# Optimization experiments

Hardware: AMD Instinct MI355X
Metric: run time of the kernel (lower is better)

The kernel has to match this reference:

```python
import jax, jax.numpy as jnp
import numpy as np

# static config (mirrors params)
T, B, NA, NF = 48, 256, 23, 4
D = NA * NF          # y_dim = 92
XD = 2               # x_dim
H = 128              # rnn_dim
HD = 128             # h_dim
NL = 2               # n_layers
FS = 0.1
BURN = 12
IN_ENC = XD + D + H  # GRU input size = 222
A0, A1 = 12, 11      # agents 0..11 -> net0, 12..22 -> net1


def setup_inputs() -> dict:
    key = jax.random.key(0)
    ks = jax.random.split(key, 16)
    s = 0.05
    rn = lambda k, shape: jax.random.normal(k, shape, jnp.float32) * s
    return {
        "states": jax.random.normal(ks[0], (T + 1, 1, B, D), jnp.float32),
        # per-network (leading dim 2) GRU layer-0 and layer-1 weights (torch GRU layout: [r|z|n])
        "W_ih0": rn(ks[1], (2, 3 * H, IN_ENC)),
        "W_hh0": rn(ks[2], (2, 3 * H, H)),
        "b_ih0": rn(ks[3], (2, 3 * H)),
        "b_hh0": rn(ks[4], (2, 3 * H)),
        "W_ih1": rn(ks[5], (2, 3 * H, H)),
        "W_hh1": rn(ks[6], (2, 3 * H, H)),
        "b_ih1": rn(ks[7], (2, 3 * H)),
        "b_hh1": rn(ks[8], (2, 3 * H)),
        # decoder MLP (dropout is identity in eval) + mean head
        "W1": rn(ks[9], (2, HD, H)),
        "b1": rn(ks[10], (2, HD)),
        "W2": rn(ks[11], (2, HD, HD)),
        "b2": rn(ks[12], (2, HD)),
        "Wm": rn(ks[13], (2, XD, HD)),
        "bm": rn(ks[14], (2, XD)),
        "rollout": 0,
        "train": 0,
    }


def _gru_cell(x, h, Wih, Whh, bih, bhh):
    gi = x @ Wih.T + bih
    gh = h @ Whh.T + bhh
    r = jax.nn.sigmoid(gi[:, :H] + gh[:, :H])
    z = jax.nn.sigmoid(gi[:, H:2 * H] + gh[:, H:2 * H])
    n = jnp.tanh(gi[:, 2 * H:] + r * gh[:, 2 * H:])
    return (1.0 - z) * n + z * h


def _batch_error(a, b):
    # sum over batch of the euclidean norm over features
    return jnp.sum(jnp.sqrt(jnp.sum((a - b) ** 2, axis=1)))


def _group_step(h, y_t, y3, y3n, lo, hi, g, P):
    # h: [NL, A*B, H]; agents lo..hi-1 of network g, folded into the batch dim
    A = hi - lo
    vel = y3[:, lo:hi, 2:4].transpose(1, 0, 2).reshape(A * B, 2)
    pos = y3[:, lo:hi, 0:2].transpose(1, 0, 2).reshape(A * B, 2)
    vel_true = y3n[:, lo:hi, 2:4].transpose(1, 0, 2).reshape(A * B, 2)
    pos_true = y3n[:, lo:hi, 0:2].transpose(1, 0, 2).reshape(A * B, 2)
    y_rep = jnp.broadcast_to(y_t[None], (A, B, D)).reshape(A * B, D)
    h_last = h[-1]
    enc_in = jnp.concatenate([vel, y_rep, h_last], axis=1)  # [A*B, IN_ENC]
    # decoder uses the PRE-update hidden state
    d = jax.nn.relu(h_last @ P["W1"][g].T + P["b1"][g])
    d = jax.nn.relu(d @ P["W2"][g].T + P["b2"][g])
    dm = d @ P["Wm"][g].T + P["bm"][g]  # [A*B, XD]
    # 2-layer GRU step
    h0n = _gru_cell(enc_in, h[0], P["W_ih0"][g], P["W_hh0"][g], P["b_ih0"][g], P["b_hh0"][g])
    h1n = _gru_cell(h0n, h[1], P["W_ih1"][g], P["W_hh1"][g], P["b_ih1"][g], P["b_hh1"][g])
    h_new = jnp.stack([h0n, h1n])
    L = _batch_error(dm, vel_true)
    ep = _batch_error(pos + vel * FS, pos_true)
    ev = _batch_error(dm[:, :2], vel_true)
    return h_new, L, ep, ev


def _forward(states, P):
    y_seq = states[:T, 0]       # [T, B, D]
    y_next = states[1:T + 1, 0]  # [T, B, D]

    def step(carry, xs):
        h0, h1, L, ep, ev = carry
        y_t, y_t1, t = xs
        y3 = y_t.reshape(B, NA, NF)
        y3n = y_t1.reshape(B, NA, NF)
        h0n, L0, ep0, ev0 = _group_step(h0, y_t, y3, y3n, 0, A0, 0, P)
        h1n, L1, ep1, ev1 = _group_step(h1, y_t, y3, y3n, A0, NA, 1, P)
        m = (t >= BURN).astype(jnp.float32)
        return (h0n, h1n, L + L0 + L1, ep + m * (ep0 + ep1), ev + m * (ev0 + ev1)), None

    init = (jnp.zeros((NL, A0 * B, H), jnp.float32),
            jnp.zeros((NL, A1 * B, H), jnp.float32),
            jnp.zeros((), jnp.float32), jnp.zeros((), jnp.float32), jnp.zeros((), jnp.float32))
    (h0, h1, L, ep, ev), _ = jax.lax.scan(step, init, (y_seq, y_next, jnp.arange(T)))
    L_rec = L / (T * NA)
    e_pos = ep / ((T - BURN) * NA)
    e_vel = ev / ((T - BURN) * NA)
    return L_rec, e_pos, e_vel


def reference(states, W_ih0, W_hh0, b_ih0, b_hh0, W_ih1, W_hh1, b_ih1, b_hh1,
              W1, b1, W2, b2, Wm, bm, rollout, train):
    P = dict(W_ih0=W_ih0, W_hh0=W_hh0, b_ih0=b_ih0, b_hh0=b_hh0,
             W_ih1=W_ih1, W_hh1=W_hh1, b_ih1=b_ih1, b_hh1=b_hh1,
             W1=W1, b1=b1, W2=W2, b2=b2, Wm=Wm, bm=bm)
    return _forward(states, P)
```

## Files before the change

kernel.cpp:

```cpp
#include <hip/hip_runtime.h>
#include <hip/hip_bf16.h>


typedef unsigned short u16;
typedef unsigned int u32;
typedef unsigned char u8;
typedef long i64;
typedef __attribute__((ext_vector_type(4))) float f32x4;

#define MFMA_F8(acc, a, b) (acc) = __builtin_amdgcn_mfma_f32_16x16x32_fp8_fp8((i64)(a), (i64)(b), (acc), 0, 0, 0)

__device__ __forceinline__ void pin(i64& x) { asm volatile("" : "+v"(x)); }

__device__ __forceinline__ u8 f2e4(float v) {
  return (u8)(__builtin_amdgcn_cvt_pk_fp8_f32(v, 0.f, 0, false) & 0xff);
}
__device__ __forceinline__ u32 pk4(float a, float b, float c, float d) {
  u32 p = (u32)__builtin_amdgcn_cvt_pk_fp8_f32(a, b, 0, false);
  return (u32)__builtin_amdgcn_cvt_pk_fp8_f32(c, d, (int)p, true);
}
__device__ __forceinline__ float sigf(float x) {
  return __builtin_amdgcn_rcpf(1.f + __expf(-x));
}
__device__ __forceinline__ float tanh_fast(float x) {
  return 1.f - 2.f * __builtin_amdgcn_rcpf(1.f + __expf(2.f * x));
}

constexpr int E0 = 2 * 384 * 352;
constexpr int E1 = E0 + 2 * 384 * 256;
constexpr int E2 = E1 + 2 * 128 * 128;
constexpr int E3 = E2 + 2 * 128 * 128;
constexpr int E4 = E3 + 2 * 128 * 128;
constexpr int E5 = E4 + 2 * 128 * 128;
constexpr int NBIAS = 2048;
constexpr int TOTAL = E5 + NBIAS + 4;
constexpr int WB_BYTE_OFF = 16384;

__global__ void prep_kernel(const float* __restrict__ Wih0, const float* __restrict__ Whh0,
                            const float* __restrict__ bih0, const float* __restrict__ bhh0,
                            const float* __restrict__ Wih1, const float* __restrict__ Whh1,
                            const float* __restrict__ bih1, const float* __restrict__ bhh1,
                            const float* __restrict__ W1, const float* __restrict__ W2,
                            u8* __restrict__ wb, float* __restrict__ wsf) {
  for (int idx = blockIdx.x * blockDim.x + threadIdx.x; idx < TOTAL;
       idx += gridDim.x * blockDim.x) {
    if (idx < E0) {
      int g = idx / 135168;
      int r = idx - g * 135168;
      int j = r / 352;
      int k = r - j * 352;
      const float* wi = Wih0 + (g * 384 + j) * 222;
      float v;
      if (k < 94) v = wi[k];
      else if (k < 96) v = 0.f;
      else if (k < 224) v = wi[k - 2];
      else v = Whh0[(g * 384 + j) * 128 + (k - 224)];
      wb[idx] = f2e4(v);
    } else if (idx < E1) {
      int q = idx - E0;
      int g = q / 98304;
      int r = q - g * 98304;
      int j = r >> 8;
      int k = r & 255;
      float v = (k < 128) ? Wih1[(g * 384 + j) * 128 + k]
                          : Whh1[(g * 384 + j) * 128 + (k - 128)];
      wb[idx] = f2e4(v);
    } else if (idx < E2) {
      int q = idx - E1; int g = q >> 14; int r = q & 16383; int j = r >> 7; int k = r & 127;
      wb[idx] = f2e4(Whh0[(g * 384 + 256 + j) * 128 + k]);
    } else if (idx < E3) {
      int q = idx - E2; int g = q >> 14; int r = q & 16383; int j = r >> 7; int k = r & 127;
      wb[idx] = f2e4(Whh1[(g * 384 + 256 + j) * 128 + k]);
    } else if (idx < E4) {
      int q = idx - E3; int g = q >> 14; int r = q & 16383; int j = r >> 7; int k = r & 127;
      wb[idx] = f2e4(W1[(g * 128 + j) * 128 + k]);
    } else if (idx < E5) {
      int q = idx - E4; int g = q >> 14; int r = q & 16383; int j = r >> 7; int k = r & 127;
      wb[idx] = f2e4(W2[(g * 128 + j) * 128 + k]);
    } else if (idx < E5 + NBIAS) {
      int q = idx - E5;
      float v;
      if (q < 512)       { int g = q >> 8, j = q & 255;              v = bih0[g*384 + j] + bhh0[g*384 + j]; }
      else if (q < 768)  { int p = q - 512;  int g = p >> 7, j = p & 127; v = bih0[g*384 + 256 + j]; }
      else if (q < 1024) { int p = q - 768;  int g = p >> 7, j = p & 127; v = bhh0[g*384 + 256 + j]; }
      else if (q < 1536) { int p = q - 1024; int g = p >> 8, j = p & 255; v = bih1[g*384 + j] + bhh1[g*384 + j]; }
      else if (q < 1792) { int p = q - 1536; int g = p >> 7, j = p & 127; v = bih1[g*384 + 256 + j]; }
      else               { int p = q - 1792; int g = p >> 7, j = p & 127; v = bhh1[g*384 + 256 + j]; }
      wsf[4 + q] = v;
    } else {
      wsf[idx - (E5 + NBIAS)] = 0.f;
    }
  }
}

__global__ __launch_bounds__(512, 2) __attribute__((amdgpu_waves_per_eu(2, 2)))
void rnn_kernel(const float* __restrict__ states,
                const u8* __restrict__ wb,
                float* __restrict__ wsf,
                const float* __restrict__ b1g,
                const float* __restrict__ b2g,
                const float* __restrict__ Wmg,
                const float* __restrict__ bmg) {
  const int blk = blockIdx.x;
  const int g = (blk < 96) ? 0 : 1;
  const int r0 = (g == 0) ? (blk * 32) : ((blk - 96) * 32);
  const int aAg = (g == 0 ? 0 : 12) + (r0 >> 8);
  const int b0 = r0 & 255;

  const int tid = threadIdx.x;
  const int wid = tid >> 6;
  const int ln = tid & 63;
  const int j_in = ln & 15;
  const int kq = ln >> 4;
  const int c0 = wid * 16 + kq * 4;
  const int jh = wid * 16 + j_in;

  __shared__ __align__(16) u8 h0b[2][32 * 136];
  __shared__ __align__(16) u8 h1b[2][32 * 136];
  __shared__ __align__(16) u8 yb[2][32 * 104];
  __shared__ __align__(16) u8 d1b[32 * 136];
  __shared__ __align__(16) u8 d2b[32 * 136];
  __shared__ __align__(16) float bias[1536];
  __shared__ float dmv[32][2];
  __shared__ float red[32][3];

  const u8* W0   = wb + g * 135168;
  const u8* W1c  = wb + E0 + g * 98304;
  const u8* Wn0p = wb + E1 + g * 16384;
  const u8* Wn1p = wb + E2 + g * 16384;
  const u8* Wm1p = wb + E3 + g * 16384;
  const u8* Wm2p = wb + E4 + g * 16384;

  i64 w0r[11], w0z[11], w0n[7];
#pragma unroll
  for (int kt = 0; kt < 11; ++kt) {
    w0r[kt] = *(const i64*)(W0 + (jh)       * 352 + kt * 32 + kq * 8);
    w0z[kt] = *(const i64*)(W0 + (128 + jh) * 352 + kt * 32 + kq * 8);
    if (kt < 7) w0n[kt] = *(const i64*)(W0 + (256 + jh) * 352 + kt * 32 + kq * 8);
  }
  i64 w1r[8], w1z[8], w1n[4];
#pragma unroll
  for (int kt = 0; kt < 8; ++kt) {
    w1r[kt] = *(const i64*)(W1c + (jh)       * 256 + kt * 32 + kq * 8);
    w1z[kt] = *(const i64*)(W1c + (128 + jh) * 256 + kt * 32 + kq * 8);
    if (kt < 4) w1n[kt] = *(const i64*)(W1c + (256 + jh) * 256 + kt * 32 + kq * 8);
  }
  i64 wn0[4], wn1[4], wm1[4], wm2[4];
#pragma unroll
  for (int kt = 0; kt < 4; ++kt) {
    wn0[kt] = *(const i64*)(Wn0p + jh * 128 + kt * 32 + kq * 8);
    wn1[kt] = *(const i64*)(Wn1p + jh * 128 + kt * 32 + kq * 8);
    wm1[kt] = *(const i64*)(Wm1p + jh * 128 + kt * 32 + kq * 8);
    wm2[kt] = *(const i64*)(Wm2p + jh * 128 + kt * 32 + kq * 8);
  }
#pragma unroll
  for (int kt = 0; kt < 11; ++kt) { pin(w0r[kt]); pin(w0z[kt]); }
#pragma unroll
  for (int kt = 0; kt < 7; ++kt) pin(w0n[kt]);
#pragma unroll
  for (int kt = 0; kt < 8; ++kt) { pin(w1r[kt]); pin(w1z[kt]); }
#pragma unroll
  for (int kt = 0; kt < 4; ++kt) {
    pin(w1n[kt]); pin(wn0[kt]); pin(wn1[kt]); pin(wm1[kt]); pin(wm2[kt]);
  }

  for (int i = tid; i < 1536; i += 512) {
    float v;
    if (i < 256)       v = wsf[4 + g * 256 + i];
    else if (i < 384)  v = wsf[516 + g * 128 + (i - 256)];
    else if (i < 512)  v = wsf[772 + g * 128 + (i - 384)];
    else if (i < 768)  v = wsf[1028 + g * 256 + (i - 512)];
    else if (i < 896)  v = wsf[1540 + g * 128 + (i - 768)];
    else if (i < 1024) v = wsf[1796 + g * 128 + (i - 896)];
    else if (i < 1152) v = b1g[g * 128 + (i - 1024)];
    else if (i < 1280) v = b2g[g * 128 + (i - 1152)];
    else               v = Wmg[g * 256 + (i - 1280)];
    bias[i] = v;
  }
  for (int i = tid; i < 32 * 136; i += 512) { h0b[0][i] = 0; h1b[0][i] = 0; }

  int sI[2], sK[2], sO0[2], sO1[2], sO2[2], sO3[2];
  bool sZ2[2], sZ3[2], sV[2];
#pragma unroll
  for (int q = 0; q < 2; ++q) {
    int idx = tid + q * 512;
    sV[q] = (idx < 768);
    int i = idx / 24, k4 = idx - i * 24;
    sI[q] = i; sK[q] = k4;
    if (k4 == 0) { sO0[q]=aAg*4+2; sO1[q]=aAg*4+3; sO2[q]=0; sO3[q]=1; sZ2[q]=false; sZ3[q]=false; }
    else {
      int kk = k4 * 4 - 2;
      sO0[q]=kk; sO1[q]=kk+1; sO2[q]=kk+2; sO3[q]=kk+3;
      sZ2[q] = (kk+2 >= 92); sZ3[q] = (kk+3 >= 92);
    }
  }
#pragma unroll
  for (int q = 0; q < 2; ++q) {
    if (sV[q]) {
      const float* srow = states + ((size_t)(b0 + sI[q])) * 92;
      float v0 = srow[sO0[q]], v1 = srow[sO1[q]];
      float v2 = sZ2[q] ? 0.f : srow[sO2[q]];
      float v3 = sZ3[q] ? 0.f : srow[sO3[q]];
      *(u32*)(&yb[0][sI[q] * 104 + sK[q] * 4]) = pk4(v0, v1, v2, v3);
    }
  }

  const float bm0 = bmg[g * 2], bm1 = bmg[g * 2 + 1];
  f32x4 hv0[2] = {{0,0,0,0},{0,0,0,0}};
  f32x4 hv1[2] = {{0,0,0,0},{0,0,0,0}};
  float accL = 0.f, accEp = 0.f, accEv = 0.f;
  __syncthreads();

  for (int t = 0; t < 48; ++t) {
    const int cur = t & 1, nxt = cur ^ 1;
    const u8* h0c = h0b[cur]; u8* h0n = h0b[nxt];
    const u8* h1c = h1b[cur]; u8* h1n = h1b[nxt];
    const u8* ybc = yb[cur];  u8* ybn = yb[nxt];

    float yv0[2], yv1[2], yv2[2], yv3[2];
#pragma unroll
    for (int q = 0; q < 2; ++q) {
      if (sV[q]) {
        const float* srow = states + ((size_t)((t + 1) * 256 + b0 + sI[q])) * 92;
        yv0[q] = srow[sO0[q]]; yv1[q] = srow[sO1[q]];
        yv2[q] = sZ2[q] ? 0.f : srow[sO2[q]];
        yv3[q] = sZ3[q] ? 0.f : srow[sO3[q]];
      }
    }

    const u8* pH1a = h1c + j_in * 136 + kq * 8;
    const u8* pH1b = h1c + (16 + j_in) * 136 + kq * 8;
    const u8* pH0a = h0c + j_in * 136 + kq * 8;
    const u8* pH0b = h0c + (16 + j_in) * 136 + kq * 8;
    const u8* pYa  = ybc + j_in * 104 + kq * 8;
    const u8* pYb  = ybc + (16 + j_in) * 104 + kq * 8;

    {
      f32x4 m0 = {0,0,0,0}, m1 = {0,0,0,0};
#pragma unroll
      for (int kt = 0; kt < 4; ++kt) {
        i64 bb0 = *(const i64*)(pH1a + kt * 32);
        i64 bb1 = *(const i64*)(pH1b + kt * 32);
        MFMA_F8(m0, wm1[kt], bb0);
        MFMA_F8(m1, wm1[kt], bb1);
      }
      f32x4 b1v = *(const f32x4*)(bias + 1024 + c0);
      *(u32*)(d1b + j_in * 136 + c0) =
        pk4(fmaxf(m0[0]+b1v[0],0.f), fmaxf(m0[1]+b1v[1],0.f), fmaxf(m0[2]+b1v[2],0.f), fmaxf(m0[3]+b1v[3],0.f));
      *(u32*)(d1b + (16 + j_in) * 136 + c0) =
        pk4(fmaxf(m1[0]+b1v[0],0.f), fmaxf(m1[1]+b1v[1],0.f), fmaxf(m1[2]+b1v[2],0.f), fmaxf(m1[3]+b1v[3],0.f));
    }

    {
      f32x4 aR[2] = {{0,0,0,0},{0,0,0,0}};
      f32x4 aZ[2] = {{0,0,0,0},{0,0,0,0}};
      f32x4 aN[2] = {{0,0,0,0},{0,0,0,0}};
      f32x4 aG[2] = {{0,0,0,0},{0,0,0,0}};
#pragma unroll
      for (int kt = 0; kt < 11; ++kt) {
        i64 bb0, bb1;
        if (kt < 3)      { bb0 = *(const i64*)(pYa + kt * 32);        bb1 = *(const i64*)(pYb + kt * 32); }
        else if (kt < 7) { bb0 = *(const i64*)(pH1a + (kt - 3) * 32); bb1 = *(const i64*)(pH1b + (kt - 3) * 32); }
        else             { bb0 = *(const i64*)(pH0a + (kt - 7) * 32); bb1 = *(const i64*)(pH0b + (kt - 7) * 32); }
        MFMA_F8(aR[0], w0r[kt], bb0); MFMA_F8(aR[1], w0r[kt], bb1);
        MFMA_F8(aZ[0], w0z[kt], bb0); MFMA_F8(aZ[1], w0z[kt], bb1);
        if (kt < 7) { MFMA_F8(aN[0], w0n[kt], bb0); MFMA_F8(aN[1], w0n[kt], bb1); }
        else        { MFMA_F8(aG[0], wn0[kt - 7], bb0); MFMA_F8(aG[1], wn0[kt - 7], bb1); }
      }
      f32x4 brv = *(const f32x4*)(bias + c0);
      f32x4 bzv = *(const f32x4*)(bias + 128 + c0);
      f32x4 biv = *(const f32x4*)(bias + 256 + c0);
      f32x4 bhv = *(const f32x4*)(bias + 384 + c0);
#pragma unroll
      for (int nt = 0; nt < 2; ++nt)
#pragma unroll
        for (int i = 0; i < 4; ++i) {
          float rv = sigf(aR[nt][i] + brv[i]);
          float zv = sigf(aZ[nt][i] + bzv[i]);
          float nv = tanh_fast(aN[nt][i] + biv[i] + rv * (aG[nt][i] + bhv[i]));
          hv0[nt][i] = (1.f - zv) * nv + zv * hv0[nt][i];
        }
#pragma unroll
      for (int nt = 0; nt < 2; ++nt)
        *(u32*)(h0n + (nt * 16 + j_in) * 136 + c0) = pk4(hv0[nt][0], hv0[nt][1], hv0[nt][2], hv0[nt][3]);
    }

    {
      int row = tid >> 4, c = (tid >> 3) & 1, part = tid & 7;
      const u8* dp = d2b + row * 136 + part * 16;
      const float* wmr = bias + 1280 + c * 128 + part * 16;
      float s = 0.f;
#pragma unroll
      for (int q = 0; q < 4; ++q) {
        u32 w = *(const u32*)(dp + q * 4);
        s += wmr[q * 4 + 0] * __builtin_amdgcn_cvt_f32_fp8((int)w, 0);
        s += wmr[q * 4 + 1] * __builtin_amdgcn_cvt_f32_fp8((int)w, 1);
        s += wmr[q * 4 + 2] * __builtin_amdgcn_cvt_f32_fp8((int)w, 2);
        s += wmr[q * 4 + 3] * __builtin_amdgcn_cvt_f32_fp8((int)w, 3);
      }
      s += __shfl_xor(s, 1); s += __shfl_xor(s, 2); s += __shfl_xor(s, 4);
      if (part == 0) dmv[row][c] = s;
    }
    __syncthreads();

    if (t > 0 && tid < 32) {
      const float* sr = states + ((size_t)((t - 1) * 256 + b0 + tid)) * 92 + aAg * 4;
      const float* sn = sr + 256 * 92;
      float dx = dmv[tid][0] + bm0 - sn[2];
      float dy = dmv[tid][1] + bm1 - sn[3];
      float e = sqrtf(dx * dx + dy * dy);
      accL += e;
      if (t - 1 >= 12) {
        accEv += e;
        float ex = sr[0] + 0.1f * sr[2] - sn[0];
        float ey = sr[1] + 0.1f * sr[3] - sn[1];
        accEp += sqrtf(ex * ex + ey * ey);
      }
    }

    {
      f32x4 m0 = {0,0,0,0}, m1 = {0,0,0,0};
#pragma unroll
      for (int kt = 0; kt < 4; ++kt) {
        i64 bb0 = *(const i64*)(d1b + j_in * 136 + kt * 32 + kq * 8);
        i64 bb1 = *(const i64*)(d1b + (16 + j_in) * 136 + kt * 32 + kq * 8);
        MFMA_F8(m0, wm2[kt], bb0);
        MFMA_F8(m1, wm2[kt], bb1);
      }
      f32x4 b2v = *(const f32x4*)(bias + 1152 + c0);
      *(u32*)(d2b + j_in * 136 + c0) =
        pk4(fmaxf(m0[0]+b2v[0],0.f), fmaxf(m0[1]+b2v[1],0.f), fmaxf(m0[2]+b2v[2],0.f), fmaxf(m0[3]+b2v[3],0.f));
      *(u32*)(d2b + (16 + j_in) * 136 + c0) =
        pk4(fmaxf(m1[0]+b2v[0],0.f), fmaxf(m1[1]+b2v[1],0.f), fmaxf(m1[2]+b2v[2],0.f), fmaxf(m1[3]+b2v[3],0.f));
    }

    {
      f32x4 aR[2] = {{0,0,0,0},{0,0,0,0}};
      f32x4 aZ[2] = {{0,0,0,0},{0,0,0,0}};
      f32x4 aN[2] = {{0,0,0,0},{0,0,0,0}};
      f32x4 aG[2] = {{0,0,0,0},{0,0,0,0}};
      const u8* pG0a = h0n + j_in * 136 + kq * 8;
      const u8* pG0b = h0n + (16 + j_in) * 136 + kq * 8;
#pragma unroll
      for (int kt = 0; kt < 8; ++kt) {
        i64 bb0, bb1;
        if (kt < 4) { bb0 = *(const i64*)(pG0a + kt * 32);        bb1 = *(const i64*)(pG0b + kt * 32); }
        else        { bb0 = *(const i64*)(pH1a + (kt - 4) * 32);  bb1 = *(const i64*)(pH1b + (kt - 4) * 32); }
        MFMA_F8(aR[0], w1r[kt], bb0); MFMA_F8(aR[1], w1r[kt], bb1);
        MFMA_F8(aZ[0], w1z[kt], bb0); MFMA_F8(aZ[1], w1z[kt], bb1);
        if (kt < 4) { MFMA_F8(aN[0], w1n[kt], bb0); MFMA_F8(aN[1], w1n[kt], bb1); }
        else        { MFMA_F8(aG[0], wn1[kt - 4], bb0); MFMA_F8(aG[1], wn1[kt - 4], bb1); }
      }
      f32x4 brv = *(const f32x4*)(bias + 512 + c0);
      f32x4 bzv = *(const f32x4*)(bias + 640 + c0);
      f32x4 biv = *(const f32x4*)(bias + 768 + c0);
      f32x4 bhv = *(const f32x4*)(bias + 896 + c0);
#pragma unroll
      for (int nt = 0; nt < 2; ++nt)
#pragma unroll
        for (int i = 0; i < 4; ++i) {
          float rv = sigf(aR[nt][i] + brv[i]);
          float zv = sigf(aZ[nt][i] + bzv[i]);
          float nv = tanh_fast(aN[nt][i] + biv[i] + rv * (aG[nt][i] + bhv[i]));
          hv1[nt][i] = (1.f - zv) * nv + zv * hv1[nt][i];
        }
#pragma unroll
      for (int nt = 0; nt < 2; ++nt)
        *(u32*)(h1n + (nt * 16 + j_in) * 136 + c0) = pk4(hv1[nt][0], hv1[nt][1], hv1[nt][2], hv1[nt][3]);
    }

#pragma unroll
    for (int q = 0; q < 2; ++q) {
      if (sV[q]) {
        *(u32*)(ybn + sI[q] * 104 + sK[q] * 4) = pk4(yv0[q], yv1[q], yv2[q], yv3[q]);
      }
    }
    __syncthreads();
  }

  {
    int row = tid >> 4, c = (tid >> 3) & 1, part = tid & 7;
    const u8* dp = d2b + row * 136 + part * 16;
    const float* wmr = bias + 1280 + c * 128 + part * 16;
    float s = 0.f;
#pragma unroll
    for (int q = 0; q < 4; ++q) {
      u32 w = *(const u32*)(dp + q * 4);
      s += wmr[q * 4 + 0] * __builtin_amdgcn_cvt_f32_fp8((int)w, 0);
      s += wmr[q * 4 + 1] * __builtin_amdgcn_cvt_f32_fp8((int)w, 1);
      s += wmr[q * 4 + 2] * __builtin_amdgcn_cvt_f32_fp8((int)w, 2);
      s += wmr[q * 4 + 3] * __builtin_amdgcn_cvt_f32_fp8((int)w, 3);
    }
    s += __shfl_xor(s, 1); s += __shfl_xor(s, 2); s += __shfl_xor(s, 4);
    if (part == 0) dmv[row][c] = s;
  }
  __syncthreads();
  if (tid < 32) {
    const float* sr = states + ((size_t)(47 * 256 + b0 + tid)) * 92 + aAg * 4;
    const float* sn = sr + 256 * 92;
    float dx = dmv[tid][0] + bm0 - sn[2];
    float dy = dmv[tid][1] + bm1 - sn[3];
    float e = sqrtf(dx * dx + dy * dy);
    accL += e;
    accEv += e;
    float ex = sr[0] + 0.1f * sr[2] - sn[0];
    float ey = sr[1] + 0.1f * sr[3] - sn[1];
    accEp += sqrtf(ex * ex + ey * ey);
    red[tid][0] = accL; red[tid][1] = accEp; red[tid][2] = accEv;
  }
  __syncthreads();
  if (tid < 3) {
    float s = 0.f;
    for (int i = 0; i < 32; ++i) s += red[i][tid];
    atomicAdd(&wsf[tid], s);
  }
}

__global__ void fin_kernel(const float* __restrict__ wacc, float* __restrict__ out) {
  if (threadIdx.x == 0 && blockIdx.x == 0) {
    out[0] = wacc[0] / 1104.f;
    out[1] = wacc[1] / 828.f;
    out[2] = wacc[2] / 828.f;
  }
}

extern "C" void kernel_launch(void* const* d_in, const int* in_sizes, int n_in,
                              void* d_out, int out_size, void* d_ws, size_t ws_size,
                              hipStream_t stream) {
  const float* states = (const float*)d_in[0];
  const float* Wih0 = (const float*)d_in[1];
  const float* Whh0 = (const float*)d_in[2];
  const float* bih0 = (const float*)d_in[3];
  const float* bhh0 = (const float*)d_in[4];
  const float* Wih1 = (const float*)d_in[5];
  const float* Whh1 = (const float*)d_in[6];
  const float* bih1 = (const float*)d_in[7];
  const float* bhh1 = (const float*)d_in[8];
  const float* W1   = (const float*)d_in[9];
  const float* b1   = (const float*)d_in[10];
  const float* W2   = (const float*)d_in[11];
  const float* b2   = (const float*)d_in[12];
  const float* Wm   = (const float*)d_in[13];
  const float* bm   = (const float*)d_in[14];

  float* wsf = (float*)d_ws;
  u8* wb = (u8*)d_ws + WB_BYTE_OFF;

  int prep_blocks = (TOTAL + 255) / 256;
  prep_kernel<<<prep_blocks, 256, 0, stream>>>(Wih0, Whh0, bih0, bhh0,
                                               Wih1, Whh1, bih1, bhh1,
                                               W1, W2, wb, wsf);
  rnn_kernel<<<184, 512, 0, stream>>>(states, wb, wsf, b1, b2, Wm, bm);
  fin_kernel<<<1, 64, 0, stream>>>(wsf, (float*)d_out);
}
```

Measured before the change: 335.5 us.

## Pre-convert states to fp8 in prep, fold per-agent x into weights, pin weights in AGPRs

The prep kernel now builds per-agent layer-0 input weights, folding the agent's x/v columns into the y columns, and converts every timestep of states to padded fp8 in global memory. The RNN kernel then loads y operands straight into registers each step instead of gathering floats into a shared y buffer. It also reuses the h1 fragments across the decoder and both GRU layers, and pins the resident weights in accumulator registers rather than VGPRs. This removes per-step shared-memory staging and the scattered float gathers, at the cost of a larger prep pass and possible AGPR-to-VGPR copies before MFMA use.

```diff
diff --git a/kernel.cpp b/kernel.cpp
--- a/kernel.cpp
+++ b/kernel.cpp
@@ -10,7 +10,7 @@
 
 #define MFMA_F8(acc, a, b) (acc) = __builtin_amdgcn_mfma_f32_16x16x32_fp8_fp8((i64)(a), (i64)(b), (acc), 0, 0, 0)
 
-__device__ __forceinline__ void pin(i64& x) { asm volatile("" : "+v"(x)); }
+__device__ __forceinline__ void pinA(i64& x) { asm volatile("" : "+a"(x)); }
 
 __device__ __forceinline__ u8 f2e4(float v) {
   return (u8)(__builtin_amdgcn_cvt_pk_fp8_f32(v, 0.f, 0, false) & 0xff);
@@ -36,13 +36,20 @@
 constexpr int TOTAL = E5 + NBIAS + 4;
 constexpr int WB_BYTE_OFF = 16384;
 
-__global__ void prep_kernel(const float* __restrict__ Wih0, const float* __restrict__ Whh0,
+constexpr int WYA_REL = E5;
+constexpr int YBG_REL = WYA_REL + 23 * 384 * 96;
+constexpr int NA1 = TOTAL;
+constexpr int NA2 = NA1 + 23 * 384 * 96;
+constexpr int NA3 = NA2 + 48 * 256 * 96;
+
+__global__ void prep_kernel(const float* __restrict__ states,
+                            const float* __restrict__ Wih0, const float* __restrict__ Whh0,
                             const float* __restrict__ bih0, const float* __restrict__ bhh0,
                             const float* __restrict__ Wih1, const float* __restrict__ Whh1,
                             const float* __restrict__ bih1, const float* __restrict__ bhh1,
                             const float* __restrict__ W1, const float* __restrict__ W2,
                             u8* __restrict__ wb, float* __restrict__ wsf) {
-  for (int idx = blockIdx.x * blockDim.x + threadIdx.x; idx < TOTAL;
+  for (int idx = blockIdx.x * blockDim.x + threadIdx.x; idx < NA3;
        idx += gridDim.x * blockDim.x) {
     if (idx < E0) {
       int g = idx / 135168;
@@ -87,8 +94,27 @@
       else if (q < 1792) { int p = q - 1536; int g = p >> 7, j = p & 127; v = bih1[g*384 + 256 + j]; }
       else               { int p = q - 1792; int g = p >> 7, j = p & 127; v = bhh1[g*384 + 256 + j]; }
       wsf[4 + q] = v;
+    } else if (idx < TOTAL) {
+      wsf[idx - (E5 + NBIAS)] = 0.f;
+    } else if (idx < NA2) {
+      int q = idx - NA1;
+      int a = q / 36864;
+      int r = q - a * 36864;
+      int j = r / 96;
+      int k = r - j * 96;
+      const float* wi = Wih0 + (((a >= 12) ? 1 : 0) * 384 + j) * 222;
+      float v = (k < 92) ? wi[2 + k] : 0.f;
+      if (k == a * 4 + 2) v += wi[0];
+      if (k == a * 4 + 3) v += wi[1];
+      wb[WYA_REL + q] = f2e4(v);
     } else {
-      wsf[idx - (E5 + NBIAS)] = 0.f;
+      int q = idx - NA2;
+      int t = q / 24576;
+      int r = q - t * 24576;
+      int row = r / 96;
+      int k = r - row * 96;
+      float v = (k < 92) ? states[((size_t)t * 256 + row) * 92 + k] : 0.f;
+      wb[YBG_REL + q] = f2e4(v);
     }
   }
 }
@@ -117,7 +143,6 @@
 
   __shared__ __align__(16) u8 h0b[2][32 * 136];
   __shared__ __align__(16) u8 h1b[2][32 * 136];
-  __shared__ __align__(16) u8 yb[2][32 * 104];
   __shared__ __align__(16) u8 d1b[32 * 136];
   __shared__ __align__(16) u8 d2b[32 * 136];
   __shared__ __align__(16) float bias[1536];
@@ -130,10 +155,18 @@
   const u8* Wn1p = wb + E2 + g * 16384;
   const u8* Wm1p = wb + E3 + g * 16384;
   const u8* Wm2p = wb + E4 + g * 16384;
+  const u8* WYA  = wb + WYA_REL + aAg * 36864;
+  const u8* YBG  = wb + YBG_REL;
 
   i64 w0r[11], w0z[11], w0n[7];
 #pragma unroll
-  for (int kt = 0; kt < 11; ++kt) {
+  for (int kt = 0; kt < 3; ++kt) {
+    w0r[kt] = *(const i64*)(WYA + (jh)       * 96 + kt * 32 + kq * 8);
+    w0z[kt] = *(const i64*)(WYA + (128 + jh) * 96 + kt * 32 + kq * 8);
+    w0n[kt] = *(const i64*)(WYA + (256 + jh) * 96 + kt * 32 + kq * 8);
+  }
+#pragma unroll
+  for (int kt = 3; kt < 11; ++kt) {
     w0r[kt] = *(const i64*)(W0 + (jh)       * 352 + kt * 32 + kq * 8);
     w0z[kt] = *(const i64*)(W0 + (128 + jh) * 352 + kt * 32 + kq * 8);
     if (kt < 7) w0n[kt] = *(const i64*)(W0 + (256 + jh) * 352 + kt * 32 + kq * 8);
@@ -154,14 +187,14 @@
     wm2[kt] = *(const i64*)(Wm2p + jh * 128 + kt * 32 + kq * 8);
   }
 #pragma unroll
-  for (int kt = 0; kt < 11; ++kt) { pin(w0r[kt]); pin(w0z[kt]); }
-#pragma unroll
-  for (int kt = 0; kt < 7; ++kt) pin(w0n[kt]);
-#pragma unroll
-  for (int kt = 0; kt < 8; ++kt) { pin(w1r[kt]); pin(w1z[kt]); }
+  for (int kt = 0; kt < 11; ++kt) { pinA(w0r[kt]); pinA(w0z[kt]); }
+#pragma unroll
+  for (int kt = 0; kt < 7; ++kt) pinA(w0n[kt]);
+#pragma unroll
+  for (int kt = 0; kt < 8; ++kt) { pinA(w1r[kt]); pinA(w1z[kt]); }
 #pragma unroll
   for (int kt = 0; kt < 4; ++kt) {
-    pin(w1n[kt]); pin(wn0[kt]); pin(wn1[kt]); pin(wm1[kt]); pin(wm2[kt]);
+    pinA(w1n[kt]); pinA(wn0[kt]); pinA(wn1[kt]); pinA(wm1[kt]); pinA(wm2[kt]);
   }
 
   for (int i = tid; i < 1536; i += 512) {
@@ -179,32 +212,6 @@
   }
   for (int i = tid; i < 32 * 136; i += 512) { h0b[0][i] = 0; h1b[0][i] = 0; }
 
-  int sI[2], sK[2], sO0[2], sO1[2], sO2[2], sO3[2];
-  bool sZ2[2], sZ3[2], sV[2];
-#pragma unroll
-  for (int q = 0; q < 2; ++q) {
-    int idx = tid + q * 512;
-    sV[q] = (idx < 768);
-    int i = idx / 24, k4 = idx - i * 24;
-    sI[q] = i; sK[q] = k4;
-    if (k4 == 0) { sO0[q]=aAg*4+2; sO1[q]=aAg*4+3; sO2[q]=0; sO3[q]=1; sZ2[q]=false; sZ3[q]=false; }
-    else {
-      int kk = k4 * 4 - 2;
-      sO0[q]=kk; sO1[q]=kk+1; sO2[q]=kk+2; sO3[q]=kk+3;
-      sZ2[q] = (kk+2 >= 92); sZ3[q] = (kk+3 >= 92);
-    }
-  }
-#pragma unroll
-  for (int q = 0; q < 2; ++q) {
-    if (sV[q]) {
-      const float* srow = states + ((size_t)(b0 + sI[q])) * 92;
-      float v0 = srow[sO0[q]], v1 = srow[sO1[q]];
-      float v2 = sZ2[q] ? 0.f : srow[sO2[q]];
-      float v3 = sZ3[q] ? 0.f : srow[sO3[q]];
-      *(u32*)(&yb[0][sI[q] * 104 + sK[q] * 4]) = pk4(v0, v1, v2, v3);
-    }
-  }
-
   const float bm0 = bmg[g * 2], bm1 = bmg[g * 2 + 1];
   f32x4 hv0[2] = {{0,0,0,0},{0,0,0,0}};
   f32x4 hv1[2] = {{0,0,0,0},{0,0,0,0}};
@@ -215,34 +222,41 @@
     const int cur = t & 1, nxt = cur ^ 1;
     const u8* h0c = h0b[cur]; u8* h0n = h0b[nxt];
     const u8* h1c = h1b[cur]; u8* h1n = h1b[nxt];
-    const u8* ybc = yb[cur];  u8* ybn = yb[nxt];
-
-    float yv0[2], yv1[2], yv2[2], yv3[2];
-#pragma unroll
-    for (int q = 0; q < 2; ++q) {
-      if (sV[q]) {
-        const float* srow = states + ((size_t)((t + 1) * 256 + b0 + sI[q])) * 92;
-        yv0[q] = srow[sO0[q]]; yv1[q] = srow[sO1[q]];
-        yv2[q] = sZ2[q] ? 0.f : srow[sO2[q]];
-        yv3[q] = sZ3[q] ? 0.f : srow[sO3[q]];
-      }
+
+    const u8* yt = YBG + t * 24576;
+    i64 yf[3][2];
+#pragma unroll
+    for (int kt = 0; kt < 3; ++kt) {
+      yf[kt][0] = *(const i64*)(yt + (b0 + j_in) * 96 + kt * 32 + kq * 8);
+      yf[kt][1] = *(const i64*)(yt + (b0 + 16 + j_in) * 96 + kt * 32 + kq * 8);
+    }
+    float sx=0, sy=0, svx=0, svy=0, nx=0, ny=0, nvx=0, nvy=0;
+    if (tid < 32) {
+      int te = (t > 0) ? (t - 1) : 0;
+      const float* sr = states + ((size_t)(te * 256 + b0 + tid)) * 92 + aAg * 4;
+      const float* sn = sr + 256 * 92;
+      sx = sr[0]; sy = sr[1]; svx = sr[2]; svy = sr[3];
+      nx = sn[0]; ny = sn[1]; nvx = sn[2]; nvy = sn[3];
     }
 
     const u8* pH1a = h1c + j_in * 136 + kq * 8;
     const u8* pH1b = h1c + (16 + j_in) * 136 + kq * 8;
     const u8* pH0a = h0c + j_in * 136 + kq * 8;
     const u8* pH0b = h0c + (16 + j_in) * 136 + kq * 8;
-    const u8* pYa  = ybc + j_in * 104 + kq * 8;
-    const u8* pYb  = ybc + (16 + j_in) * 104 + kq * 8;
+
+    i64 fh1[4][2];
+#pragma unroll
+    for (int kt = 0; kt < 4; ++kt) {
+      fh1[kt][0] = *(const i64*)(pH1a + kt * 32);
+      fh1[kt][1] = *(const i64*)(pH1b + kt * 32);
+    }
 
     {
       f32x4 m0 = {0,0,0,0}, m1 = {0,0,0,0};
 #pragma unroll
       for (int kt = 0; kt < 4; ++kt) {
-        i64 bb0 = *(const i64*)(pH1a + kt * 32);
-        i64 bb1 = *(const i64*)(pH1b + kt * 32);
-        MFMA_F8(m0, wm1[kt], bb0);
-        MFMA_F8(m1, wm1[kt], bb1);
+        MFMA_F8(m0, wm1[kt], fh1[kt][0]);
+        MFMA_F8(m1, wm1[kt], fh1[kt][1]);
       }
       f32x4 b1v = *(const f32x4*)(bias + 1024 + c0);
       *(u32*)(d1b + j_in * 136 + c0) =
@@ -259,9 +273,10 @@
 #pragma unroll
       for (int kt = 0; kt < 11; ++kt) {
         i64 bb0, bb1;
-        if (kt < 3)      { bb0 = *(const i64*)(pYa + kt * 32);        bb1 = *(const i64*)(pYb + kt * 32); }
-        else if (kt < 7) { bb0 = *(const i64*)(pH1a + (kt - 3) * 32); bb1 = *(const i64*)(pH1b + (kt - 3) * 32); }
-        else             { bb0 = *(const i64*)(pH0a + (kt - 7) * 32); bb1 = *(const i64*)(pH0b + (kt - 7) * 32); }
+        if (kt < 3)      { bb0 = yf[kt][0];      bb1 = yf[kt][1]; }
+        else if (kt < 7) { bb0 = fh1[kt - 3][0]; bb1 = fh1[kt - 3][1]; }
+        else             { bb0 = *(const i64*)(pH0a + (kt - 7) * 32);
+                           bb1 = *(const i64*)(pH0b + (kt - 7) * 32); }
         MFMA_F8(aR[0], w0r[kt], bb0); MFMA_F8(aR[1], w0r[kt], bb1);
         MFMA_F8(aZ[0], w0z[kt], bb0); MFMA_F8(aZ[1], w0z[kt], bb1);
         if (kt < 7) { MFMA_F8(aN[0], w0n[kt], bb0); MFMA_F8(aN[1], w0n[kt], bb1); }
@@ -304,16 +319,14 @@
     __syncthreads();
 
     if (t > 0 && tid < 32) {
-      const float* sr = states + ((size_t)((t - 1) * 256 + b0 + tid)) * 92 + aAg * 4;
-      const float* sn = sr + 256 * 92;
-      float dx = dmv[tid][0] + bm0 - sn[2];
-      float dy = dmv[tid][1] + bm1 - sn[3];
+      float dx = dmv[tid][0] + bm0 - nvx;
+      float dy = dmv[tid][1] + bm1 - nvy;
       float e = sqrtf(dx * dx + dy * dy);
       accL += e;
       if (t - 1 >= 12) {
         accEv += e;
-        float ex = sr[0] + 0.1f * sr[2] - sn[0];
-        float ey = sr[1] + 0.1f * sr[3] - sn[1];
+        float ex = sx + 0.1f * svx - nx;
+        float ey = sy + 0.1f * svy - ny;
         accEp += sqrtf(ex * ex + ey * ey);
       }
     }
@@ -344,8 +357,8 @@
 #pragma unroll
       for (int kt = 0; kt < 8; ++kt) {
         i64 bb0, bb1;
-        if (kt < 4) { bb0 = *(const i64*)(pG0a + kt * 32);        bb1 = *(const i64*)(pG0b + kt * 32); }
-        else        { bb0 = *(const i64*)(pH1a + (kt - 4) * 32);  bb1 = *(const i64*)(pH1b + (kt - 4) * 32); }
+        if (kt < 4) { bb0 = *(const i64*)(pG0a + kt * 32); bb1 = *(const i64*)(pG0b + kt * 32); }
+        else        { bb0 = fh1[kt - 4][0];                bb1 = fh1[kt - 4][1]; }
         MFMA_F8(aR[0], w1r[kt], bb0); MFMA_F8(aR[1], w1r[kt], bb1);
         MFMA_F8(aZ[0], w1z[kt], bb0); MFMA_F8(aZ[1], w1z[kt], bb1);
         if (kt < 4) { MFMA_F8(aN[0], w1n[kt], bb0); MFMA_F8(aN[1], w1n[kt], bb1); }
@@ -367,13 +380,6 @@
 #pragma unroll
       for (int nt = 0; nt < 2; ++nt)
         *(u32*)(h1n + (nt * 16 + j_in) * 136 + c0) = pk4(hv1[nt][0], hv1[nt][1], hv1[nt][2], hv1[nt][3]);
-    }
-
-#pragma unroll
-    for (int q = 0; q < 2; ++q) {
-      if (sV[q]) {
-        *(u32*)(ybn + sI[q] * 104 + sK[q] * 4) = pk4(yv0[q], yv1[q], yv2[q], yv3[q]);
-      }
     }
     __syncthreads();
   }
@@ -446,8 +452,9 @@
   float* wsf = (float*)d_ws;
   u8* wb = (u8*)d_ws + WB_BYTE_OFF;
 
-  int prep_blocks = (TOTAL + 255) / 256;
-  prep_kernel<<<prep_blocks, 256, 0, stream>>>(Wih0, Whh0, bih0, bhh0,
+  int prep_blocks = (NA3 + 255) / 256;
+  if (prep_blocks > 2048) prep_blocks = 2048;
+  prep_kernel<<<prep_blocks, 256, 0, stream>>>(states, Wih0, Whh0, bih0, bhh0,
                                                Wih1, Whh1, bih1, bhh1,
                                                W1, W2, wb, wsf);
   rnn_kernel<<<184, 512, 0, stream>>>(states, wb, wsf, b1, b2, Wm, bm);
```

Result: no change. 338.3 us (+0.8%).
